# Kernel tuning notes

Hardware: AMD Instinct MI355X
Metric: run time of the kernel (lower is better)

## Reference

```python
import jax, jax.numpy as jnp
import numpy as np
from jax import lax

EPS = 1e-8

def squash(x, axis=-1):
    sq = jnp.sum(x * x, axis=axis, keepdims=True)
    return sq / (1.0 + sq) * x / (jnp.sqrt(sq) + EPS)

def setup_inputs() -> dict:
    key = jax.random.key(0)
    ks = jax.random.split(key, 12)
    B = 512
    x = jax.random.normal(ks[0], (B, 1, 28, 28), dtype=jnp.float32)
    conv1_w = 0.05 * jax.random.normal(ks[1], (256, 1, 9, 9), dtype=jnp.float32)
    conv1_b = jnp.zeros((256,), dtype=jnp.float32)
    prim_w = 0.01 * jax.random.normal(ks[2], (256, 256, 9, 9), dtype=jnp.float32)
    prim_b = jnp.zeros((256,), dtype=jnp.float32)
    # DigitCaps W: (out_caps=10, in_caps=1152, out_dim=16, in_dim=8)
    W_digit = 0.01 * jax.random.normal(ks[3], (10, 1152, 16, 8), dtype=jnp.float32)
    dec_w1 = 0.05 * jax.random.normal(ks[4], (512, 160), dtype=jnp.float32)
    dec_b1 = jnp.zeros((512,), dtype=jnp.float32)
    dec_w2 = 0.05 * jax.random.normal(ks[5], (1024, 512), dtype=jnp.float32)
    dec_b2 = jnp.zeros((1024,), dtype=jnp.float32)
    dec_w3 = 0.05 * jax.random.normal(ks[6], (784, 1024), dtype=jnp.float32)
    dec_b3 = jnp.zeros((784,), dtype=jnp.float32)
    return {"x": x, "conv1_w": conv1_w, "conv1_b": conv1_b,
            "prim_w": prim_w, "prim_b": prim_b, "W_digit": W_digit,
            "dec_w1": dec_w1, "dec_b1": dec_b1, "dec_w2": dec_w2,
            "dec_b2": dec_b2, "dec_w3": dec_w3, "dec_b3": dec_b3}

def reference(x, conv1_w, conv1_b, prim_w, prim_b, W_digit,
              dec_w1, dec_b1, dec_w2, dec_b2, dec_w3, dec_b3):
    NUM_ROUTING = 3
    # conv1 + relu: [B,1,28,28] -> [B,256,20,20]
    out = lax.conv(x, conv1_w, (1, 1), 'VALID') + conv1_b[None, :, None, None]
    out = jax.nn.relu(out)
    # primary caps conv: -> [B,256,6,6]
    out = lax.conv(out, prim_w, (2, 2), 'VALID') + prim_b[None, :, None, None]
    N, C, H, W = out.shape
    # [B,32,8,6,6] -> [B,32,6,6,8] -> [B,1152,8]
    out = out.reshape(N, 32, 8, H, W).transpose(0, 1, 3, 4, 2).reshape(N, -1, 8)
    u = squash(out)
    # u_hat: [B, out_caps=10, in_caps=1152, out_dim=16]
    u_hat = jnp.einsum('ocdi,bci->bocd', W_digit, u)
    tu = lax.stop_gradient(u_hat)
    b = jnp.zeros((N, 10, 1152, 1), dtype=u_hat.dtype)
    for _ in range(NUM_ROUTING - 1):
        c = jax.nn.softmax(b, axis=1)
        s = jnp.sum(c * tu, axis=2)            # [B,10,16]
        v = squash(s)
        b = b + jnp.einsum('bocd,bod->boc', tu, v)[..., None]
    c = jax.nn.softmax(b, axis=1)
    s = jnp.sum(c * u_hat, axis=2)
    v = squash(s)                               # [B,10,16]
    logits = jnp.linalg.norm(v, axis=-1)        # [B,10]
    pred = jax.nn.one_hot(jnp.argmax(logits, axis=1), 10, dtype=v.dtype)  # [B,10]
    masked = (v * pred[..., None]).reshape(N, -1)  # [B,160]
    h = jax.nn.relu(masked @ dec_w1.T + dec_b1)
    h = jax.nn.relu(h @ dec_w2.T + dec_b2)
    reconstruction = jax.nn.sigmoid(h @ dec_w3.T + dec_b3)  # [B,784]
    return (logits, reconstruction)
```

## Files before the change

### kernel.cpp

```cpp
#include <hip/hip_runtime.h>
#include <math.h>

typedef unsigned short u16;
typedef unsigned int u32;
typedef __attribute__((ext_vector_type(4))) float f32x4;
typedef __attribute__((ext_vector_type(4))) u32 u32x4;
typedef __attribute__((ext_vector_type(8))) short s16x8;
typedef __attribute__((ext_vector_type(8))) u16 u16x8;
typedef __attribute__((ext_vector_type(4))) u16 u16x4;

__device__ __forceinline__ float bf2f(u16 h) { return __uint_as_float(((u32)h) << 16); }
__device__ __forceinline__ u16 f2bf(float f) {
    u32 u = __float_as_uint(f);
    return (u16)((u + 0x7FFFu + ((u >> 16) & 1u)) >> 16);
}
__device__ __forceinline__ void unpack8(u16x8 a, float* f) {
    const u32* p = (const u32*)&a;
#pragma unroll
    for (int k = 0; k < 4; ++k) {
        u32 w = p[k];
        f[2 * k] = __uint_as_float(w << 16);
        f[2 * k + 1] = __uint_as_float(w & 0xffff0000u);
    }
}

#define OFF_CONV1 0ull
#define OFF_CP    104857600ull
#define OFF_UHAT  0ull
#define OFF_U     188743680ull
#define OFF_WR    198180864ull
#define OFF_WB    208797696ull
#define OFF_W1T   211746816ull
#define OFF_MASK  211829760ull
#define OFF_H1    212157440ull
#define OFF_H2    213206016ull

#define GLDS16(SRC, DST) __builtin_amdgcn_global_load_lds( \
    (const __attribute__((address_space(1))) unsigned int*)(SRC), \
    (__attribute__((address_space(3))) unsigned int*)(DST), 16, 0, 0)

__global__ __launch_bounds__(256) void k_prep(const float* __restrict__ cw,
                                              float* __restrict__ w1t,
                                              const float* __restrict__ wdig,
                                              u16* __restrict__ wb,
                                              const float* __restrict__ pw,
                                              u16* __restrict__ wrq) {
    __shared__ u16 ld[128 * 82];
    int bid = blockIdx.x, t = threadIdx.x;
    if (bid < 81) {
        w1t[bid * 256 + t] = cw[t * 81 + bid];
    } else if (bid < 801) {
        int i = ((bid - 81) * 256 + t) * 8;
        u16x8 r;
#pragma unroll
        for (int j = 0; j < 8; ++j) r[j] = f2bf(wdig[i + j]);
        *(u16x8*)&wb[i] = r;
    } else {
        int och = bid - 801;
        const float* src = pw + (size_t)och * 20736;
        u16* dst = wrq + (size_t)och * 20736;
        for (int half = 0; half < 2; ++half) {
            const float* s2 = src + half * 128 * 81;
            for (int i = t; i < 128 * 81; i += 256) {
                int ic = i / 81, kk = i - ic * 81;
                ld[ic * 82 + kk] = f2bf(s2[i]);
            }
            __syncthreads();
            int col = t & 127, kh = t >> 7;
            for (int kk = kh; kk < 81; kk += 2)
                dst[kk * 256 + half * 128 + col] = ld[col * 82 + kk];
            __syncthreads();
        }
    }
}

__global__ __launch_bounds__(256) void k_conv1(const float* __restrict__ x,
                                               const float* __restrict__ w1t,
                                               const float* __restrict__ bias,
                                               u16* __restrict__ out) {
    int b = blockIdx.x / 20, y = blockIdx.x % 20, t = threadIdx.x;
    __shared__ float xs[252];
    if (t < 252) xs[t] = x[b * 784 + y * 28 + t];
    __syncthreads();
    float acc[20];
#pragma unroll
    for (int i = 0; i < 20; ++i) acc[i] = 0.f;
#pragma unroll
    for (int ky = 0; ky < 9; ++ky) {
        float xr[28];
#pragma unroll
        for (int i = 0; i < 28; ++i) xr[i] = xs[ky * 28 + i];
#pragma unroll
        for (int kx = 0; kx < 9; ++kx) {
            float wv = w1t[(ky * 9 + kx) * 256 + t];
#pragma unroll
            for (int ox = 0; ox < 20; ++ox) acc[ox] += wv * xr[ox + kx];
        }
    }
    float bv = bias[t];
    u16* op = out + ((size_t)(b * 20 + y) * 20) * 256 + t;
#pragma unroll
    for (int ox = 0; ox < 20; ++ox) {
        float f = fmaxf(acc[ox] + bv, 0.f);
        op[ox * 256] = f2bf(f);
    }
}

__global__ __launch_bounds__(256) void k_gemm(const u16* __restrict__ wr,
                                              const u16* __restrict__ cin,
                                              u16* __restrict__ cp16) {
    __shared__ __align__(16) u16 Al[128 * 64];
    __shared__ __align__(16) u16 Bl[128 * 64];
    int tid = threadIdx.x, lane = tid & 63, w = tid >> 6;
    int pix0 = blockIdx.x * 128, och0 = blockIdx.y * 128, q = blockIdx.z;
    int kbase = q * 5184;
    int slot = lane & 7;
    const char* ab[4];
    const char* bb[4];
#pragma unroll
    for (int j = 0; j < 4; ++j) {
        int r = w * 32 + j * 8 + (lane >> 3);
        int sl = slot ^ (r & 7);
        ab[j] = (const char*)wr + (size_t)(och0 + r) * 41472 + sl * 16;
        int p = pix0 + r, bi = p / 36, rr = p % 36, yy = rr / 6, xx = rr % 6;
        bb[j] = (const char*)cin + (size_t)((bi * 20 + 2 * yy) * 20 + 2 * xx) * 512 + sl * 16;
    }
    f32x4 acc[4][4];
#pragma unroll
    for (int i = 0; i < 4; ++i)
#pragma unroll
        for (int j = 0; j < 4; ++j) acc[i][j] = (f32x4){0.f, 0.f, 0.f, 0.f};
    int wm = (w & 1) * 64, wn = (w >> 1) * 64;

    for (int it = 0; it < 81; ++it) {
        int kk0 = kbase + it * 64;
        int kykx = kk0 >> 8, ic0 = kk0 & 255;
        int aoffu = kk0 * 2;
        int boffu = ((kykx / 9) * 20 + (kykx % 9)) * 512 + ic0 * 2;
#pragma unroll
        for (int j = 0; j < 4; ++j) {
            GLDS16(ab[j] + aoffu, &Al[(w * 32 + j * 8) * 64]);
            GLDS16(bb[j] + boffu, &Bl[(w * 32 + j * 8) * 64]);
        }
        __syncthreads();
#pragma unroll
        for (int s = 0; s < 2; ++s) {
            s16x8 af[4], bf[4];
#pragma unroll
            for (int f = 0; f < 4; ++f) {
                int m = wm + f * 16 + (lane & 15);
                int ch = ((s << 2) + (lane >> 4)) ^ (m & 7);
                af[f] = *(const s16x8*)&Al[m * 64 + ch * 8];
                int n = wn + f * 16 + (lane & 15);
                int ch2 = ((s << 2) + (lane >> 4)) ^ (n & 7);
                bf[f] = *(const s16x8*)&Bl[n * 64 + ch2 * 8];
            }
#pragma unroll
            for (int fm = 0; fm < 4; ++fm)
#pragma unroll
                for (int fn = 0; fn < 4; ++fn)
                    acc[fm][fn] = __builtin_amdgcn_mfma_f32_16x16x32_bf16(
                        af[fm], bf[fn], acc[fm][fn], 0, 0, 0);
        }
        __syncthreads();
    }
#pragma unroll
    for (int fm = 0; fm < 4; ++fm) {
        int och = och0 + wm + fm * 16 + (lane >> 4) * 4;
#pragma unroll
        for (int fn = 0; fn < 4; ++fn) {
            int pix = pix0 + wn + fn * 16 + (lane & 15);
            u16x4 r;
#pragma unroll
            for (int i = 0; i < 4; ++i) r[i] = f2bf(acc[fm][fn][i]);
            *(u16x4*)&cp16[(((size_t)q * 18432 + pix) << 8) + och] = r;
        }
    }
}

__global__ void k_squash(const u16* __restrict__ cp16, const float* __restrict__ pbias,
                         u16* __restrict__ u) {
    int idx = blockIdx.x * 256 + threadIdx.x;
    int pix = idx >> 5, g = idx & 31;
    size_t base = ((size_t)pix << 8) + g * 8;
    float s[8];
#pragma unroll
    for (int i = 0; i < 8; ++i) s[i] = pbias[g * 8 + i];
#pragma unroll
    for (int q = 0; q < 4; ++q) {
        u16x8 a = *(const u16x8*)&cp16[q * 4718592ull + base];
        float f[8];
        unpack8(a, f);
#pragma unroll
        for (int i = 0; i < 8; ++i) s[i] += f[i];
    }
    float sq = 0.f;
#pragma unroll
    for (int i = 0; i < 8; ++i) sq += s[i] * s[i];
    float scale = (sq / (1.f + sq)) / (sqrtf(sq) + 1e-8f);
    int b = pix / 36, cap = g * 36 + pix % 36;
    u16x8 r;
#pragma unroll
    for (int i = 0; i < 8; ++i) r[i] = f2bf(s[i] * scale);
    *(u16x8*)&u[((size_t)b * 1152 + cap) * 8] = r;
}

__global__ __launch_bounds__(256) void k_uhat(const u16* __restrict__ u,
                                              const u16* __restrict__ wb,
                                              u32* __restrict__ uhp) {
    int o = blockIdx.x, cg = blockIdx.y, bq = blockIdx.z, t = threadIdx.x;
    __shared__ __align__(16) u16 wl[64 * 136];
    const u16* wsrc = wb + ((size_t)o * 1152 + cg * 64) * 128;
    for (int i = t; i < 1024; i += 256) {
        int row = i >> 4, j = i & 15;
        *(u16x8*)&wl[row * 136 + j * 8] = *(const u16x8*)&wsrc[i * 8];
    }
    __syncthreads();
    int bl = t >> 5, c2l = t & 31;
    const u16* w0p = &wl[(2 * c2l) * 136];
    const u16* w1p = &wl[(2 * c2l + 1) * 136];
    for (int bt = bq * 16; bt < bq * 16 + 16; ++bt) {
        int b = bt * 8 + bl;
        const u16x8* up = (const u16x8*)(u + ((size_t)b * 1152 + cg * 64 + 2 * c2l) * 8);
        float u0[8], u1[8];
        unpack8(up[0], u0);
        unpack8(up[1], u1);
        u32 outv[16];
#pragma unroll
        for (int d = 0; d < 16; ++d) {
            u16x8 wv0 = *(const u16x8*)&w0p[d * 8];
            u16x8 wv1 = *(const u16x8*)&w1p[d * 8];
            float w0f[8], w1f[8];
            unpack8(wv0, w0f);
            unpack8(wv1, w1f);
            float dA = 0.f, dB = 0.f;
#pragma unroll
            for (int i = 0; i < 8; ++i) {
                dA += w0f[i] * u0[i];
                dB += w1f[i] * u1[i];
            }
            outv[d] = (u32)f2bf(dA) | ((u32)f2bf(dB) << 16);
        }
        u32* dst = uhp + (size_t)b * 92160 + (cg * 32 + c2l) * 160 + o * 16;
#pragma unroll
        for (int k = 0; k < 4; ++k)
            *(u32x4*)&dst[k * 4] = *(u32x4*)&outv[k * 4];
    }
}

__global__ __launch_bounds__(256, 2) void k_routing(const u32* __restrict__ uhp,
                                                    float* __restrict__ logits,
                                                    float* __restrict__ masked) {
    int b = blockIdx.x, t = threadIdx.x;
    __shared__ float blog[10][1160];
    __shared__ __align__(16) u32 chunk[32 * 164];
    __shared__ float cwl[10][66];
    __shared__ float v[160];
    __shared__ float lg[10];
    __shared__ int am;
    for (int i = t; i < 11600; i += 256) ((float*)blog)[i] = 0.f;
    const u32* uh = uhp + (size_t)b * 92160;
    int o16 = t >> 4, d16 = t & 15;
    float s = 0.f;
    __syncthreads();

    if (t < 160) {
        const u32* p = uh + t;
#pragma unroll 8
        for (int c2 = 0; c2 < 576; ++c2) {
            u32 wv = p[c2 * 160];
            s += bf2f((u16)(wv & 0xffffu)) + bf2f((u16)(wv >> 16));
        }
        s *= 0.1f;
        float sq = s * s;
        sq += __shfl_xor(sq, 1, 16);
        sq += __shfl_xor(sq, 2, 16);
        sq += __shfl_xor(sq, 4, 16);
        sq += __shfl_xor(sq, 8, 16);
        float scale = (sq / (1.f + sq)) / (sqrtf(sq) + 1e-8f);
        v[t] = s * scale;
    }
    __syncthreads();

    for (int pass = 1; pass < 3; ++pass) {
        float snew = 0.f;
        for (int cg = 0; cg < 18; ++cg) {
            const u32x4* src4 = (const u32x4*)(uh + (size_t)cg * 5120);
#pragma unroll
            for (int k = 0; k < 5; ++k) {
                int idx4 = t + k * 256;
                int c2l = idx4 / 40, j4 = idx4 - c2l * 40;
                ((u32x4*)chunk)[c2l * 41 + j4] = src4[idx4];
            }
            __syncthreads();
#pragma unroll
            for (int jj = 0; jj < 2; ++jj) {
                int idx = t + jj * 256;
                if (idx < 320) {
                    int c2l = idx / 10, o = idx - c2l * 10;
                    const u32* row = &chunk[c2l * 164 + o * 16];
                    const float* vp = &v[o * 16];
                    float d0 = 0.f, d1 = 0.f;
#pragma unroll
                    for (int d = 0; d < 16; ++d) {
                        u32 wv = row[d];
                        float vv = vp[d];
                        d0 += __uint_as_float(wv << 16) * vv;
                        d1 += __uint_as_float(wv & 0xffff0000u) * vv;
                    }
                    int c2 = cg * 32 + c2l;
                    blog[o][2 * c2] += d0;
                    blog[o][2 * c2 + 1] += d1;
                }
            }
            __syncthreads();
            if (t < 64) {
                int c = cg * 64 + t;
                float bb[10], mx = -1e30f;
#pragma unroll
                for (int o = 0; o < 10; ++o) { bb[o] = blog[o][c]; mx = fmaxf(mx, bb[o]); }
                float sum = 0.f;
#pragma unroll
                for (int o = 0; o < 10; ++o) { bb[o] = __expf(bb[o] - mx); sum += bb[o]; }
                float rs = 1.f / sum;
#pragma unroll
                for (int o = 0; o < 10; ++o) cwl[o][t] = bb[o] * rs;
            }
            __syncthreads();
            if (t < 160) {
                const u32* col = &chunk[t];
                const float* cwp = &cwl[o16][0];
#pragma unroll 8
                for (int c2l = 0; c2l < 32; ++c2l) {
                    u32 wv = col[c2l * 164];
                    snew += __uint_as_float(wv << 16) * cwp[2 * c2l] +
                            __uint_as_float(wv & 0xffff0000u) * cwp[2 * c2l + 1];
                }
            }
            __syncthreads();
        }
        if (t < 160) {
            s = snew;
            float sq = s * s;
            sq += __shfl_xor(sq, 1, 16);
            sq += __shfl_xor(sq, 2, 16);
            sq += __shfl_xor(sq, 4, 16);
            sq += __shfl_xor(sq, 8, 16);
            float scale = (sq / (1.f + sq)) / (sqrtf(sq) + 1e-8f);
            v[t] = s * scale;
            if (d16 == 0 && pass == 2) {
                float sn = sqrtf(sq);
                float l = (sq / (1.f + sq)) * (sn / (sn + 1e-8f));
                lg[o16] = l;
                logits[b * 10 + o16] = l;
            }
        }
        __syncthreads();
    }
    if (t == 0) {
        float best = lg[0];
        int bi = 0;
#pragma unroll
        for (int o = 1; o < 10; ++o)
            if (lg[o] > best) { best = lg[o]; bi = o; }
        am = bi;
    }
    __syncthreads();
    if (t < 160) masked[b * 160 + t] = (o16 == am) ? v[t] : 0.f;
}

template <int TB, int K, int OUTDIM, int ACT>
__global__ __launch_bounds__(256) void k_dec(const float* __restrict__ in,
                                             const float* __restrict__ W,
                                             const float* __restrict__ bias,
                                             float* __restrict__ out) {
    int bt = blockIdx.y * TB;
    int o = blockIdx.x * 256 + threadIdx.x;
    __shared__ float ins[TB * K];
    for (int i = threadIdx.x; i < TB * K; i += 256) ins[i] = in[(size_t)bt * K + i];
    __syncthreads();
    if (o < OUTDIM) {
        float acc[TB];
#pragma unroll
        for (int bb = 0; bb < TB; ++bb) acc[bb] = 0.f;
        const float* wr = W + (size_t)o * K;
#pragma unroll 4
        for (int k = 0; k < K; ++k) {
            float wv = wr[k];
#pragma unroll
            for (int bb = 0; bb < TB; ++bb) acc[bb] += wv * ins[bb * K + k];
        }
        float bv = bias[o];
#pragma unroll
        for (int bb = 0; bb < TB; ++bb) {
            float z = acc[bb] + bv;
            float r = (ACT == 0) ? fmaxf(z, 0.f) : 1.f / (1.f + __expf(-z));
            out[(size_t)(bt + bb) * OUTDIM + o] = r;
        }
    }
}

extern "C" void kernel_launch(void* const* d_in, const int* in_sizes, int n_in,
                              void* d_out, int out_size, void* d_ws, size_t ws_size,
                              hipStream_t stream) {
    const float* x       = (const float*)d_in[0];
    const float* conv1_w = (const float*)d_in[1];
    const float* conv1_b = (const float*)d_in[2];
    const float* prim_w  = (const float*)d_in[3];
    const float* prim_b  = (const float*)d_in[4];
    const float* W_digit = (const float*)d_in[5];
    const float* dec_w1  = (const float*)d_in[6];
    const float* dec_b1  = (const float*)d_in[7];
    const float* dec_w2  = (const float*)d_in[8];
    const float* dec_b2  = (const float*)d_in[9];
    const float* dec_w3  = (const float*)d_in[10];
    const float* dec_b3  = (const float*)d_in[11];

    char* ws = (char*)d_ws;
    u16*   conv1o = (u16*)(ws + OFF_CONV1);
    u16*   cp16   = (u16*)(ws + OFF_CP);
    u32*   uhat   = (u32*)(ws + OFF_UHAT);
    u16*   u      = (u16*)(ws + OFF_U);
    u16*   wrq    = (u16*)(ws + OFF_WR);
    u16*   wb     = (u16*)(ws + OFF_WB);
    float* w1t    = (float*)(ws + OFF_W1T);
    float* maskd  = (float*)(ws + OFF_MASK);
    float* h1     = (float*)(ws + OFF_H1);
    float* h2     = (float*)(ws + OFF_H2);
    float* logits = (float*)d_out;
    float* recon  = (float*)d_out + 5120;

    k_prep<<<dim3(1057), dim3(256), 0, stream>>>(conv1_w, w1t, W_digit, wb, prim_w, wrq);
    k_conv1<<<dim3(10240), dim3(256), 0, stream>>>(x, w1t, conv1_b, conv1o);
    k_gemm<<<dim3(144, 2, 4), dim3(256), 0, stream>>>(wrq, conv1o, cp16);
    k_squash<<<dim3(2304), dim3(256), 0, stream>>>(cp16, prim_b, u);
    k_uhat<<<dim3(10, 18, 4), dim3(256), 0, stream>>>(u, wb, uhat);
    k_routing<<<dim3(512), dim3(256), 0, stream>>>(uhat, logits, maskd);
    k_dec<4, 160, 512, 0><<<dim3(2, 128), dim3(256), 0, stream>>>(maskd, dec_w1, dec_b1, h1);
    k_dec<8, 512, 1024, 0><<<dim3(4, 64), dim3(256), 0, stream>>>(h1, dec_w2, dec_b2, h2);
    k_dec<8, 1024, 784, 1><<<dim3(4, 64), dim3(256), 0, stream>>>(h2, dec_w3, dec_b3, recon);
}
```

Measured before the change: 723.8 us.

## Run conv1 on bf16 MFMA and fuse first routing sum into u_hat kernel

conv1 becomes an implicit GEMM using 16x16x32 bf16 MFMA. Weights are padded to K=96 in a prep step, and each block handles a whole image with input converted to bf16 in LDS. The u_hat kernel also reduces the per-capsule-group sums used in the first routing pass and writes them into reused workspace, so routing no longer rescans all of u_hat for the initial s. The risks are bf16 rounding of the input and the conv1 weights, and reuse of the wrq buffer region for the partial sums after the GEMM has consumed it.

```diff
diff --git a/kernel.cpp b/kernel.cpp
--- a/kernel.cpp
+++ b/kernel.cpp
@@ -30,7 +30,7 @@
 #define OFF_U     188743680ull
 #define OFF_WR    198180864ull
 #define OFF_WB    208797696ull
-#define OFF_W1T   211746816ull
+#define OFF_WC2   211746816ull
 #define OFF_MASK  211829760ull
 #define OFF_H1    212157440ull
 #define OFF_H2    213206016ull
@@ -40,23 +40,21 @@
     (__attribute__((address_space(3))) unsigned int*)(DST), 16, 0, 0)
 
 __global__ __launch_bounds__(256) void k_prep(const float* __restrict__ cw,
-                                              float* __restrict__ w1t,
+                                              u16* __restrict__ wc2,
                                               const float* __restrict__ wdig,
                                               u16* __restrict__ wb,
                                               const float* __restrict__ pw,
                                               u16* __restrict__ wrq) {
     __shared__ u16 ld[128 * 82];
     int bid = blockIdx.x, t = threadIdx.x;
-    if (bid < 81) {
-        w1t[bid * 256 + t] = cw[t * 81 + bid];
-    } else if (bid < 801) {
-        int i = ((bid - 81) * 256 + t) * 8;
+    if (bid < 720) {
+        int i = (bid * 256 + t) * 8;
         u16x8 r;
 #pragma unroll
         for (int j = 0; j < 8; ++j) r[j] = f2bf(wdig[i + j]);
         *(u16x8*)&wb[i] = r;
-    } else {
-        int och = bid - 801;
+    } else if (bid < 976) {
+        int och = bid - 720;
         const float* src = pw + (size_t)och * 20736;
         u16* dst = wrq + (size_t)och * 20736;
         for (int half = 0; half < 2; ++half) {
@@ -71,38 +69,59 @@
                 dst[kk * 256 + half * 128 + col] = ld[col * 82 + kk];
             __syncthreads();
         }
+    } else {
+        for (int k = 0; k < 96; ++k)
+            wc2[t * 96 + k] = (k < 81) ? f2bf(cw[t * 81 + k]) : (u16)0;
     }
 }
 
 __global__ __launch_bounds__(256) void k_conv1(const float* __restrict__ x,
-                                               const float* __restrict__ w1t,
+                                               const u16* __restrict__ wc2,
                                                const float* __restrict__ bias,
                                                u16* __restrict__ out) {
-    int b = blockIdx.x / 20, y = blockIdx.x % 20, t = threadIdx.x;
-    __shared__ float xs[252];
-    if (t < 252) xs[t] = x[b * 784 + y * 28 + t];
+    int b = blockIdx.x, tid = threadIdx.x, lane = tid & 63, w = tid >> 6;
+    __shared__ u16 xsb[784];
+    __shared__ float bs[256];
+    bs[tid] = bias[tid];
+    for (int i = tid; i < 784; i += 256) xsb[i] = f2bf(x[b * 784 + i]);
     __syncthreads();
-    float acc[20];
-#pragma unroll
-    for (int i = 0; i < 20; ++i) acc[i] = 0.f;
-#pragma unroll
-    for (int ky = 0; ky < 9; ++ky) {
-        float xr[28];
-#pragma unroll
-        for (int i = 0; i < 28; ++i) xr[i] = xs[ky * 28 + i];
-#pragma unroll
-        for (int kx = 0; kx < 9; ++kx) {
-            float wv = w1t[(ky * 9 + kx) * 256 + t];
-#pragma unroll
-            for (int ox = 0; ox < 20; ++ox) acc[ox] += wv * xr[ox + kx];
-        }
-    }
-    float bv = bias[t];
-    u16* op = out + ((size_t)(b * 20 + y) * 20) * 256 + t;
-#pragma unroll
-    for (int ox = 0; ox < 20; ++ox) {
-        float f = fmaxf(acc[ox] + bv, 0.f);
-        op[ox * 256] = f2bf(f);
+    int wm = w * 64, l15 = lane & 15, lh = lane >> 4;
+    s16x8 afr[3][4];
+#pragma unroll
+    for (int s = 0; s < 3; ++s)
+#pragma unroll
+        for (int f = 0; f < 4; ++f)
+            afr[s][f] = *(const s16x8*)&wc2[(wm + f * 16 + l15) * 96 + s * 32 + lh * 8];
+    int off[24];
+#pragma unroll
+    for (int s = 0; s < 3; ++s)
+#pragma unroll
+        for (int j = 0; j < 8; ++j) {
+            int k = s * 32 + lh * 8 + j;
+            off[s * 8 + j] = (k < 81) ? ((k / 9) * 28 + (k % 9)) : 0;
+        }
+    for (int nt = 0; nt < 25; ++nt) {
+        int p = nt * 16 + l15;
+        int base = (p / 20) * 28 + (p % 20);
+        s16x8 bfr[3];
+#pragma unroll
+        for (int s = 0; s < 3; ++s) {
+#pragma unroll
+            for (int j = 0; j < 8; ++j)
+                bfr[s][j] = (short)xsb[base + off[s * 8 + j]];
+        }
+#pragma unroll
+        for (int f = 0; f < 4; ++f) {
+            f32x4 acc = (f32x4){0.f, 0.f, 0.f, 0.f};
+#pragma unroll
+            for (int s = 0; s < 3; ++s)
+                acc = __builtin_amdgcn_mfma_f32_16x16x32_bf16(afr[s][f], bfr[s], acc, 0, 0, 0);
+            int och = wm + f * 16 + lh * 4;
+            u16x4 r;
+#pragma unroll
+            for (int i = 0; i < 4; ++i) r[i] = f2bf(fmaxf(acc[i] + bs[och + i], 0.f));
+            *(u16x4*)&out[((size_t)b * 400 + p) * 256 + och] = r;
+        }
     }
 }
 
@@ -207,7 +226,8 @@
 
 __global__ __launch_bounds__(256) void k_uhat(const u16* __restrict__ u,
                                               const u16* __restrict__ wb,
-                                              u32* __restrict__ uhp) {
+                                              u32* __restrict__ uhp,
+                                              float* __restrict__ s0p) {
     int o = blockIdx.x, cg = blockIdx.y, bq = blockIdx.z, t = threadIdx.x;
     __shared__ __align__(16) u16 wl[64 * 136];
     const u16* wsrc = wb + ((size_t)o * 1152 + cg * 64) * 128;
@@ -226,6 +246,7 @@
         unpack8(up[0], u0);
         unpack8(up[1], u1);
         u32 outv[16];
+        float sd[16];
 #pragma unroll
         for (int d = 0; d < 16; ++d) {
             u16x8 wv0 = *(const u16x8*)&w0p[d * 8];
@@ -240,15 +261,26 @@
                 dB += w1f[i] * u1[i];
             }
             outv[d] = (u32)f2bf(dA) | ((u32)f2bf(dB) << 16);
-        }
-        u32* dst = uhp + (size_t)b * 92160 + (cg * 32 + c2l) * 160 + o * 16;
+            sd[d] = dA + dB;
+        }
+#pragma unroll
+        for (int m = 1; m < 32; m <<= 1)
+#pragma unroll
+            for (int d = 0; d < 16; ++d) sd[d] += __shfl_xor(sd[d], m, 32);
+        if (c2l == 0) {
+            float* dst = s0p + ((size_t)cg * 512 + b) * 160 + o * 16;
+#pragma unroll
+            for (int d = 0; d < 16; ++d) dst[d] = sd[d];
+        }
+        u32* dstv = uhp + (size_t)b * 92160 + (cg * 32 + c2l) * 160 + o * 16;
 #pragma unroll
         for (int k = 0; k < 4; ++k)
-            *(u32x4*)&dst[k * 4] = *(u32x4*)&outv[k * 4];
+            *(u32x4*)&dstv[k * 4] = *(u32x4*)&outv[k * 4];
     }
 }
 
 __global__ __launch_bounds__(256, 2) void k_routing(const u32* __restrict__ uhp,
+                                                    const float* __restrict__ s0p,
                                                     float* __restrict__ logits,
                                                     float* __restrict__ masked) {
     int b = blockIdx.x, t = threadIdx.x;
@@ -262,15 +294,11 @@
     const u32* uh = uhp + (size_t)b * 92160;
     int o16 = t >> 4, d16 = t & 15;
     float s = 0.f;
-    __syncthreads();
 
     if (t < 160) {
-        const u32* p = uh + t;
-#pragma unroll 8
-        for (int c2 = 0; c2 < 576; ++c2) {
-            u32 wv = p[c2 * 160];
-            s += bf2f((u16)(wv & 0xffffu)) + bf2f((u16)(wv >> 16));
-        }
+#pragma unroll
+        for (int cg = 0; cg < 18; ++cg)
+            s += s0p[((size_t)cg * 512 + b) * 160 + t];
         s *= 0.1f;
         float sq = s * s;
         sq += __shfl_xor(sq, 1, 16);
@@ -422,20 +450,21 @@
     u32*   uhat   = (u32*)(ws + OFF_UHAT);
     u16*   u      = (u16*)(ws + OFF_U);
     u16*   wrq    = (u16*)(ws + OFF_WR);
+    float* s0p    = (float*)(ws + OFF_WR);
     u16*   wb     = (u16*)(ws + OFF_WB);
-    float* w1t    = (float*)(ws + OFF_W1T);
+    u16*   wc2    = (u16*)(ws + OFF_WC2);
     float* maskd  = (float*)(ws + OFF_MASK);
     float* h1     = (float*)(ws + OFF_H1);
     float* h2     = (float*)(ws + OFF_H2);
     float* logits = (float*)d_out;
     float* recon  = (float*)d_out + 5120;
 
-    k_prep<<<dim3(1057), dim3(256), 0, stream>>>(conv1_w, w1t, W_digit, wb, prim_w, wrq);
-    k_conv1<<<dim3(10240), dim3(256), 0, stream>>>(x, w1t, conv1_b, conv1o);
+    k_prep<<<dim3(977), dim3(256), 0, stream>>>(conv1_w, wc2, W_digit, wb, prim_w, wrq);
+    k_conv1<<<dim3(512), dim3(256), 0, stream>>>(x, wc2, conv1_b, conv1o);
     k_gemm<<<dim3(144, 2, 4), dim3(256), 0, stream>>>(wrq, conv1o, cp16);
     k_squash<<<dim3(2304), dim3(256), 0, stream>>>(cp16, prim_b, u);
-    k_uhat<<<dim3(10, 18, 4), dim3(256), 0, stream>>>(u, wb, uhat);
-    k_routing<<<dim3(512), dim3(256), 0, stream>>>(uhat, logits, maskd);
+    k_uhat<<<dim3(10, 18, 4), dim3(256), 0, stream>>>(u, wb, uhat, s0p);
+    k_routing<<<dim3(512), dim3(256), 0, stream>>>(uhat, s0p, logits, maskd);
     k_dec<4, 160, 512, 0><<<dim3(2, 128), dim3(256), 0, stream>>>(maskd, dec_w1, dec_b1, h1);
     k_dec<8, 512, 1024, 0><<<dim3(4, 64), dim3(256), 0, stream>>>(h1, dec_w2, dec_b2, h2);
     k_dec<8, 1024, 784, 1><<<dim3(4, 64), dim3(256), 0, stream>>>(h2, dec_w3, dec_b3, recon);
```

Measured after the change: 700.7 us. 3.2% less time.
